# Kernel optimization log

Hardware: AMD Instinct MI355X
Metric: run time of the kernel (lower is better)

## Reference

```python
import jax, jax.numpy as jnp
import numpy as np

N_NODES = 100000

def _graph_conv(x, src, dst, W, b, activation=None):
    # DGL GraphConv with norm='both':
    #   h = D_in^{-1/2} * A^T * (D_out^{-1/2} * x) @ W + b
    n = x.shape[0]
    ones = jnp.ones(src.shape[0], dtype=x.dtype)
    deg_out = jax.ops.segment_sum(ones, src, num_segments=n)
    deg_in = jax.ops.segment_sum(ones, dst, num_segments=n)
    norm_src = jax.lax.rsqrt(jnp.maximum(deg_out, 1.0))  # [N]
    norm_dst = jax.lax.rsqrt(jnp.maximum(deg_in, 1.0))   # [N]
    h = x * norm_src[:, None]
    # DGL applies W before aggregation when out_feats <= in_feats (cheaper messages)
    if W.shape[1] <= W.shape[0]:
        h = h @ W
        agg = jax.ops.segment_sum(h[src], dst, num_segments=n)
    else:
        agg = jax.ops.segment_sum(h[src], dst, num_segments=n)
        agg = agg @ W
    out = agg * norm_dst[:, None] + b
    if activation is not None:
        out = activation(out)
    return out

def setup_inputs() -> dict:
    key = jax.random.key(0)
    k1, k2, k3, k4 = jax.random.split(key, 4)
    in_f, hid_f, out_f = 128, 128, 64
    n_edges = 3200000
    x = jax.random.normal(k1, (N_NODES, in_f), dtype=jnp.float32)
    edge_index = jax.random.randint(k2, (2, n_edges), 0, N_NODES, dtype=jnp.int64)
    W0 = jax.random.normal(k3, (in_f, hid_f), dtype=jnp.float32) / np.sqrt(in_f)
    b0 = jnp.zeros((hid_f,), dtype=jnp.float32)
    W1 = jax.random.normal(k4, (hid_f, out_f), dtype=jnp.float32) / np.sqrt(hid_f)
    b1 = jnp.zeros((out_f,), dtype=jnp.float32)
    return {"x": x, "edge_index": edge_index, "W0": W0, "b0": b0, "W1": W1, "b1": b1}

def reference(x, edge_index, W0, b0, W1, b1):
    src, dst = edge_index[0], edge_index[1]
    h = _graph_conv(x, src, dst, W0, b0, activation=jax.nn.relu)  # gn0: in->hidden, relu
    out = _graph_conv(h, src, dst, W1, b1, activation=None)       # gn1: hidden->out
    return out
```

## Files before the change

kernel.cpp:

```cpp
#include <hip/hip_runtime.h>
#include <hip/hip_bf16.h>


typedef unsigned short u16;
typedef unsigned int   u32;
using bf16x8 = __attribute__((ext_vector_type(8))) short;
using f32x4  = __attribute__((ext_vector_type(4))) float;

__device__ __forceinline__ float bfu2f(u16 u) {
    union { unsigned int i; float f; } c; c.i = ((unsigned int)u) << 16; return c.f;
}
__device__ __forceinline__ u16 f2bfu(float f) {
    union { float fv; unsigned int i; } c; c.fv = f;
    unsigned int x = c.i;
    x += 0x7fffu + ((x >> 16) & 1u);
    return (u16)(x >> 16);
}

constexpr int NCHUNK = 128;

__global__ __launch_bounds__(1024) void hist8_kernel(const int* __restrict__ src,
    const int* __restrict__ dst, int E, int M, u32* __restrict__ pd, u32* __restrict__ ps)
{
    __shared__ u32 h[25088];
    const int W = (M + 3) >> 2;
    const bool isSrc = blockIdx.x >= NCHUNK;
    const int c = isSrc ? (blockIdx.x - NCHUNK) : blockIdx.x;
    const int* vals = isSrc ? src : dst;
    u32* out = (isSrc ? ps : pd) + (size_t)c * W;
    for (int k = threadIdx.x; k < W; k += 1024) h[k] = 0;
    __syncthreads();
    const int ebeg = (int)((long long)c * E / NCHUNK);
    const int eend = (int)((long long)(c + 1) * E / NCHUNK);
    for (int i = ebeg + threadIdx.x; i < eend; i += 1024) {
        int v = vals[i];
        atomicAdd(&h[v >> 2], 1u << ((v & 3) * 8));
    }
    __syncthreads();
    for (int k = threadIdx.x; k < W; k += 1024) out[k] = h[k];
}

__global__ __launch_bounds__(256) void cumreduce_kernel(const u32* __restrict__ pd,
    const u32* __restrict__ ps, u32* __restrict__ cum, int* __restrict__ deg_in,
    float* __restrict__ ns, float* __restrict__ nd, int* __restrict__ bsum, int M)
{
    __shared__ int sh[256];
    const int W = (M + 3) >> 2;
    int w = blockIdx.x * 256 + threadIdx.x;
    u32 run = 0, so = 0;
    if (w < W) {
        for (int c = 0; c < NCHUNK; ++c) {
            cum[(size_t)c * W + w] = run;
            run += pd[(size_t)c * W + w];
        }
        for (int c = 0; c < NCHUNK; ++c) so += ps[(size_t)c * W + w];
        #pragma unroll
        for (int j = 0; j < 4; ++j) {
            int d = w * 4 + j;
            if (d < M) {
                int din  = (run >> (j * 8)) & 255;
                int dout = (so  >> (j * 8)) & 255;
                deg_in[d] = din;
                nd[d] = rsqrtf((float)max(din, 1));
                ns[d] = rsqrtf((float)max(dout, 1));
            }
        }
    }
    sh[threadIdx.x] = (run & 255) + ((run >> 8) & 255) + ((run >> 16) & 255) + (run >> 24);
    __syncthreads();
    for (int off = 128; off > 0; off >>= 1) {
        if (threadIdx.x < off) sh[threadIdx.x] += sh[threadIdx.x + off];
        __syncthreads();
    }
    if (threadIdx.x == 0) bsum[blockIdx.x] = sh[0];
}

__global__ __launch_bounds__(256) void scan2_kernel(const int* __restrict__ bsum,
    int* __restrict__ boff, int NB, int* __restrict__ row_ptr, int M)
{
    __shared__ int sh[256];
    const int t = threadIdx.x;
    sh[t] = (t < NB) ? bsum[t] : 0;
    __syncthreads();
    for (int off = 1; off < 256; off <<= 1) {
        int v = (t >= off) ? sh[t - off] : 0;
        __syncthreads();
        sh[t] += v;
        __syncthreads();
    }
    if (t < NB) boff[t] = (t == 0) ? 0 : sh[t - 1];
    if (t == 0) row_ptr[M] = sh[255];
}

__global__ __launch_bounds__(256) void scan3_kernel(const int* __restrict__ deg,
    const int* __restrict__ boff, int* __restrict__ row_ptr, int M)
{
    __shared__ int sh[256];
    const int base = blockIdx.x * 1024;
    const int idx0 = base + threadIdx.x * 4;
    int v[4]; int s = 0;
    #pragma unroll
    for (int j = 0; j < 4; ++j) {
        int i = idx0 + j;
        v[j] = (i < M) ? deg[i] : 0;
        s += v[j];
    }
    sh[threadIdx.x] = s;
    __syncthreads();
    for (int off = 1; off < 256; off <<= 1) {
        int t = (threadIdx.x >= off) ? sh[threadIdx.x - off] : 0;
        __syncthreads();
        sh[threadIdx.x] += t;
        __syncthreads();
    }
    int run = boff[blockIdx.x] + ((threadIdx.x == 0) ? 0 : sh[threadIdx.x - 1]);
    #pragma unroll
    for (int j = 0; j < 4; ++j) {
        int i = idx0 + j;
        if (i < M) { row_ptr[i] = run; run += v[j]; }
    }
}

constexpr int NS = 8;
__global__ __launch_bounds__(256) void place2_kernel(const int* __restrict__ src,
    const int* __restrict__ dst, int E, int M, const int* __restrict__ row_ptr,
    const u32* __restrict__ cum, int* __restrict__ eidx)
{
    __shared__ u32 rank[3200];
    const int W = (M + 3) >> 2;
    const int r = blockIdx.x >> 7;
    const int c = blockIdx.x & 127;
    const int span = (M + NS - 1) / NS;
    const int lo = r * span;
    const int hi = min(lo + span, M);
    const int wspan = (span + 3) >> 2;
    for (int k = threadIdx.x; k < wspan; k += 256) rank[k] = 0;
    __syncthreads();
    const int ebeg = (int)((long long)c * E / NCHUNK);
    const int eend = (int)((long long)(c + 1) * E / NCHUNK);
    const u32* cumc = cum + (size_t)c * W;
    for (int i = ebeg + threadIdx.x; i < eend; i += 256) {
        int d = dst[i];
        if (d >= lo && d < hi) {
            int dl = d - lo;
            u32 old = atomicAdd(&rank[dl >> 2], 1u << ((dl & 3) * 8));
            int rk   = (old >> ((dl & 3) * 8)) & 255;
            int base = (cumc[d >> 2] >> ((d & 3) * 8)) & 255;
            eidx[row_ptr[d] + base + rk] = src[i];
        }
    }
}

__global__ __launch_bounds__(256) void transpose_kernel(const float* __restrict__ W0,
    const float* __restrict__ W1, u16* __restrict__ Wt0, u16* __restrict__ Wt1)
{
    __shared__ float t[32][33];
    int b = blockIdx.x;
    const float* in; u16* out; int K, N, tk, tn;
    if (b < 16) { in = W0; out = Wt0; K = 128; N = 128; tk = b >> 2; tn = b & 3; }
    else { b -= 16; in = W1; out = Wt1; K = 128; N = 64; tk = b >> 1; tn = b & 1; }
    int tx = threadIdx.x & 31, ty = threadIdx.x >> 5;
    int k0 = tk * 32, n0 = tn * 32;
    #pragma unroll
    for (int i = 0; i < 4; ++i)
        t[ty + 8 * i][tx] = in[(size_t)(k0 + ty + 8 * i) * N + n0 + tx];
    __syncthreads();
    #pragma unroll
    for (int i = 0; i < 4; ++i)
        out[(size_t)(n0 + ty + 8 * i) * K + k0 + tx] = f2bfu(t[tx][ty + 8 * i]);
}

template<int NOUT, bool XF32>
__global__ __launch_bounds__(256) void mfma_gemm_kernel(const void* __restrict__ xin,
    const u16* __restrict__ Wt, const float* __restrict__ rowscale,
    u16* __restrict__ out, int M)
{
    constexpr int CPW = NOUT / 64;
    __shared__ __align__(16) u16 xs[64 * 128];
    __shared__ __align__(16) u16 wl[NOUT * 128];

    const int tid = threadIdx.x;
    const int w = tid >> 6;
    const int l = tid & 63;
    const int ln = l & 15, g = l >> 4;
    const int rbase = blockIdx.x * 64;

    for (int c = tid; c < NOUT * 16; c += 256) {
        int n = c >> 4, s = c & 15;
        uint4 v = *(const uint4*)(Wt + (size_t)n * 128 + s * 8);
        *(uint4*)(&wl[n * 128 + ((s * 8) ^ ((n & 7) << 3))]) = v;
    }
    if (XF32) {
        const float* xf = (const float*)xin;
        for (int c = tid; c < 64 * 16; c += 256) {
            int r = c >> 4, s = c & 15;
            int row = rbase + r;
            uint4 p = make_uint4(0, 0, 0, 0);
            if (row < M) {
                float sc = rowscale[row];
                float4 v0 = *(const float4*)(xf + (size_t)row * 128 + s * 8);
                float4 v1 = *(const float4*)(xf + (size_t)row * 128 + s * 8 + 4);
                p.x = ((u32)f2bfu(v0.y * sc) << 16) | f2bfu(v0.x * sc);
                p.y = ((u32)f2bfu(v0.w * sc) << 16) | f2bfu(v0.z * sc);
                p.z = ((u32)f2bfu(v1.y * sc) << 16) | f2bfu(v1.x * sc);
                p.w = ((u32)f2bfu(v1.w * sc) << 16) | f2bfu(v1.z * sc);
            }
            *(uint4*)(&xs[r * 128 + ((s * 8) ^ ((r & 7) << 3))]) = p;
        }
    } else {
        const u16* xb = (const u16*)xin;
        for (int c = tid; c < 64 * 16; c += 256) {
            int r = c >> 4, s = c & 15;
            int row = rbase + r;
            uint4 v = make_uint4(0, 0, 0, 0);
            if (row < M) v = *(const uint4*)(xb + (size_t)row * 128 + s * 8);
            *(uint4*)(&xs[r * 128 + ((s * 8) ^ ((r & 7) << 3))]) = v;
        }
    }
    __syncthreads();

    bf16x8 bfrag[CPW][4];
    #pragma unroll
    for (int cf = 0; cf < CPW; ++cf) {
        int n = (w * CPW + cf) * 16 + ln;
        #pragma unroll
        for (int ks = 0; ks < 4; ++ks) {
            int koff = ks * 32 + g * 8;
            bfrag[cf][ks] = *(const bf16x8*)(&wl[n * 128 + (koff ^ ((n & 7) << 3))]);
        }
    }

    f32x4 acc[4][CPW];
    #pragma unroll
    for (int m = 0; m < 4; ++m)
        #pragma unroll
        for (int cf = 0; cf < CPW; ++cf)
            acc[m][cf] = (f32x4){0.f, 0.f, 0.f, 0.f};

    #pragma unroll
    for (int m = 0; m < 4; ++m) {
        int r = m * 16 + ln;
        #pragma unroll
        for (int ks = 0; ks < 4; ++ks) {
            int koff = ks * 32 + g * 8;
            bf16x8 a = *(const bf16x8*)(&xs[r * 128 + (koff ^ ((ln & 7) << 3))]);
            #pragma unroll
            for (int cf = 0; cf < CPW; ++cf)
                acc[m][cf] = __builtin_amdgcn_mfma_f32_16x16x32_bf16(
                    a, bfrag[cf][ks], acc[m][cf], 0, 0, 0);
        }
    }

    #pragma unroll
    for (int m = 0; m < 4; ++m) {
        int row = rbase + m * 16 + g * 4;
        #pragma unroll
        for (int j = 0; j < 4; ++j) {
            if (row + j < M) {
                #pragma unroll
                for (int cf = 0; cf < CPW; ++cf) {
                    int col = (w * CPW + cf) * 16 + ln;
                    out[(size_t)(row + j) * NOUT + col] = f2bfu(acc[m][cf][j]);
                }
            }
        }
    }
}

__global__ __launch_bounds__(256) void gather128_kernel(const int* __restrict__ row_ptr,
    const int* __restrict__ eidx, const u16* __restrict__ h,
    const float* __restrict__ nd, const float* __restrict__ nsc,
    const float* __restrict__ b, u16* __restrict__ out, int M)
{
    const int wave = (blockIdx.x * 256 + threadIdx.x) >> 6;
    const int lane = threadIdx.x & 63;
    if (wave >= M) return;
    const int beg = row_ptr[wave];
    const int end = row_ptr[wave + 1];
    const int half = lane >> 5;
    const int l = lane & 31;
    float a0 = 0.f, a1 = 0.f, a2 = 0.f, a3 = 0.f;
    for (int jb = beg; jb < end; jb += 64) {
        const int cnt = min(64, end - jb);
        int myidx = (jb + lane < end) ? eidx[jb + lane] : 0;
        int k = 0;
        for (; k + 8 <= cnt; k += 8) {
            int s0 = __shfl(myidx, k + 0 + half);
            int s1 = __shfl(myidx, k + 2 + half);
            int s2 = __shfl(myidx, k + 4 + half);
            int s3 = __shfl(myidx, k + 6 + half);
            ushort4 u0 = *(const ushort4*)(h + (size_t)s0 * 128 + l * 4);
            ushort4 u1 = *(const ushort4*)(h + (size_t)s1 * 128 + l * 4);
            ushort4 u2 = *(const ushort4*)(h + (size_t)s2 * 128 + l * 4);
            ushort4 u3 = *(const ushort4*)(h + (size_t)s3 * 128 + l * 4);
            a0 += (bfu2f(u0.x) + bfu2f(u1.x)) + (bfu2f(u2.x) + bfu2f(u3.x));
            a1 += (bfu2f(u0.y) + bfu2f(u1.y)) + (bfu2f(u2.y) + bfu2f(u3.y));
            a2 += (bfu2f(u0.z) + bfu2f(u1.z)) + (bfu2f(u2.z) + bfu2f(u3.z));
            a3 += (bfu2f(u0.w) + bfu2f(u1.w)) + (bfu2f(u2.w) + bfu2f(u3.w));
        }
        for (; k < cnt; k += 2) {
            int kk = k + half;
            int s = __shfl(myidx, (kk < cnt) ? kk : 0);
            ushort4 u = *(const ushort4*)(h + (size_t)s * 128 + l * 4);
            if (kk < cnt) {
                a0 += bfu2f(u.x); a1 += bfu2f(u.y);
                a2 += bfu2f(u.z); a3 += bfu2f(u.w);
            }
        }
    }
    a0 += __shfl_xor(a0, 32); a1 += __shfl_xor(a1, 32);
    a2 += __shfl_xor(a2, 32); a3 += __shfl_xor(a3, 32);
    if (half == 0) {
        const float s = nd[wave];
        const float sn = nsc[wave];
        ushort4 o;
        o.x = f2bfu(fmaxf(fmaf(a0, s, b[l * 4 + 0]), 0.f) * sn);
        o.y = f2bfu(fmaxf(fmaf(a1, s, b[l * 4 + 1]), 0.f) * sn);
        o.z = f2bfu(fmaxf(fmaf(a2, s, b[l * 4 + 2]), 0.f) * sn);
        o.w = f2bfu(fmaxf(fmaf(a3, s, b[l * 4 + 3]), 0.f) * sn);
        *(ushort4*)(out + (size_t)wave * 128 + l * 4) = o;
    }
}

__global__ __launch_bounds__(256) void gather64_kernel(const int* __restrict__ row_ptr,
    const int* __restrict__ eidx, const u16* __restrict__ h,
    const float* __restrict__ nd, const float* __restrict__ b,
    float* __restrict__ out, int M)
{
    const int wave = (blockIdx.x * 256 + threadIdx.x) >> 6;
    const int lane = threadIdx.x & 63;
    if (wave >= M) return;
    const int beg = row_ptr[wave];
    const int end = row_ptr[wave + 1];
    const int quad = lane >> 4;
    const int l = lane & 15;
    float a0 = 0.f, a1 = 0.f, a2 = 0.f, a3 = 0.f;
    for (int jb = beg; jb < end; jb += 64) {
        const int cnt = min(64, end - jb);
        int myidx = (jb + lane < end) ? eidx[jb + lane] : 0;
        int k = 0;
        for (; k + 16 <= cnt; k += 16) {
            int s0 = __shfl(myidx, k + 0 + quad);
            int s1 = __shfl(myidx, k + 4 + quad);
            int s2 = __shfl(myidx, k + 8 + quad);
            int s3 = __shfl(myidx, k + 12 + quad);
            ushort4 u0 = *(const ushort4*)(h + (size_t)s0 * 64 + l * 4);
            ushort4 u1 = *(const ushort4*)(h + (size_t)s1 * 64 + l * 4);
            ushort4 u2 = *(const ushort4*)(h + (size_t)s2 * 64 + l * 4);
            ushort4 u3 = *(const ushort4*)(h + (size_t)s3 * 64 + l * 4);
            a0 += (bfu2f(u0.x) + bfu2f(u1.x)) + (bfu2f(u2.x) + bfu2f(u3.x));
            a1 += (bfu2f(u0.y) + bfu2f(u1.y)) + (bfu2f(u2.y) + bfu2f(u3.y));
            a2 += (bfu2f(u0.z) + bfu2f(u1.z)) + (bfu2f(u2.z) + bfu2f(u3.z));
            a3 += (bfu2f(u0.w) + bfu2f(u1.w)) + (bfu2f(u2.w) + bfu2f(u3.w));
        }
        for (; k < cnt; k += 4) {
            int kk = k + quad;
            int s = __shfl(myidx, (kk < cnt) ? kk : 0);
            ushort4 u = *(const ushort4*)(h + (size_t)s * 64 + l * 4);
            if (kk < cnt) {
                a0 += bfu2f(u.x); a1 += bfu2f(u.y);
                a2 += bfu2f(u.z); a3 += bfu2f(u.w);
            }
        }
    }
    a0 += __shfl_xor(a0, 32); a1 += __shfl_xor(a1, 32);
    a2 += __shfl_xor(a2, 32); a3 += __shfl_xor(a3, 32);
    a0 += __shfl_xor(a0, 16); a1 += __shfl_xor(a1, 16);
    a2 += __shfl_xor(a2, 16); a3 += __shfl_xor(a3, 16);
    if (quad == 0) {
        const float s = nd[wave];
        float4 o;
        o.x = fmaf(a0, s, b[l * 4 + 0]);
        o.y = fmaf(a1, s, b[l * 4 + 1]);
        o.z = fmaf(a2, s, b[l * 4 + 2]);
        o.w = fmaf(a3, s, b[l * 4 + 3]);
        *(float4*)(out + (size_t)wave * 64 + l * 4) = o;
    }
}

extern "C" void kernel_launch(void* const* d_in, const int* in_sizes, int n_in,
                              void* d_out, int out_size, void* d_ws, size_t ws_size,
                              hipStream_t stream) {
    const float* x  = (const float*)d_in[0];
    const int*   ei = (const int*)d_in[1];
    const float* W0 = (const float*)d_in[2];
    const float* b0 = (const float*)d_in[3];
    const float* W1 = (const float*)d_in[4];
    const float* b1 = (const float*)d_in[5];

    const int M = in_sizes[0] / 128;
    const int E = in_sizes[1] / 2;
    const int* src = ei;
    const int* dst = ei + E;
    const int W = (M + 3) >> 2;

    char* ws = (char*)d_ws;
    size_t off = 0;
    auto alloc = [&](size_t bytes) {
        void* p = ws + off; off += (bytes + 255) & ~(size_t)255; return p;
    };
    int*   deg_in   = (int*)  alloc((size_t)M * 4);
    float* norm_src = (float*)alloc((size_t)M * 4);
    float* norm_dst = (float*)alloc((size_t)M * 4);
    int*   row_ptr  = (int*)  alloc((size_t)(M + 1) * 4);
    int*   bsum     = (int*)  alloc(256 * 4);
    int*   boff     = (int*)  alloc(256 * 4);
    u16*   Wt0      = (u16*)  alloc(128 * 128 * 2);
    u16*   Wt1      = (u16*)  alloc(64 * 128 * 2);
    int*   eidx     = (int*)  alloc((size_t)E * 4);
    u16*   hbuf     = (u16*)  alloc((size_t)M * 128 * 2);
    u16*   out0b    = (u16*)  alloc((size_t)M * 128 * 2);

    u32* pd  = (u32*)hbuf;
    u32* ps  = pd + (size_t)NCHUNK * W;
    u32* cum = ps + (size_t)NCHUNK * W;

    const int NB = (M + 1023) / 1024;

    hist8_kernel<<<2 * NCHUNK, 1024, 0, stream>>>(src, dst, E, M, pd, ps);
    cumreduce_kernel<<<NB, 256, 0, stream>>>(pd, ps, cum, deg_in,
        norm_src, norm_dst, bsum, M);
    scan2_kernel<<<1, 256, 0, stream>>>(bsum, boff, NB, row_ptr, M);
    scan3_kernel<<<NB, 256, 0, stream>>>(deg_in, boff, row_ptr, M);
    place2_kernel<<<8 * NCHUNK, 256, 0, stream>>>(src, dst, E, M, row_ptr, cum, eidx);
    transpose_kernel<<<24, 256, 0, stream>>>(W0, W1, Wt0, Wt1);

    const int GB = (M + 63) / 64;
    mfma_gemm_kernel<128, true><<<GB, 256, 0, stream>>>(x, Wt0, norm_src, hbuf, M);
    gather128_kernel<<<(M * 64 + 255) / 256, 256, 0, stream>>>(
        row_ptr, eidx, hbuf, norm_dst, norm_src, b0, out0b, M);

    mfma_gemm_kernel<64, false><<<GB, 256, 0, stream>>>(out0b, Wt1, nullptr, hbuf, M);
    gather64_kernel<<<(M * 64 + 255) / 256, 256, 0, stream>>>(
        row_ptr, eidx, hbuf, norm_dst, b1, (float*)d_out, M);
}
```

Before: 309.3 us.

## Widen gather loads to 16-byte bf16x8 and halve place2 destination splits

The two gather kernels now load eight bf16 values per lane as uint4 instead of four as ushort4, so each wave handles twice as many edges per iteration. Each thread keeps eight fp32 accumulators, with an extra shuffle-reduction level at the end. Separately, place2 cuts the destination-range splits from 8 to 4, doubling its LDS rank array, and reorders block-to-chunk mapping so adjacent blocks share edge chunks. The aim is more memory-level parallelism and fewer redundant edge scans, at the cost of more registers and LDS, which may lower occupancy.

```diff
diff --git a/kernel.cpp b/kernel.cpp
--- a/kernel.cpp
+++ b/kernel.cpp
@@ -15,6 +15,17 @@
     unsigned int x = c.i;
     x += 0x7fffu + ((x >> 16) & 1u);
     return (u16)(x >> 16);
+}
+__device__ __forceinline__ void acc8(float* a, uint4 u) {
+    union { u32 i; float f; } c;
+    c.i = u.x << 16;         a[0] += c.f;
+    c.i = u.x & 0xffff0000u; a[1] += c.f;
+    c.i = u.y << 16;         a[2] += c.f;
+    c.i = u.y & 0xffff0000u; a[3] += c.f;
+    c.i = u.z << 16;         a[4] += c.f;
+    c.i = u.z & 0xffff0000u; a[5] += c.f;
+    c.i = u.w << 16;         a[6] += c.f;
+    c.i = u.w & 0xffff0000u; a[7] += c.f;
 }
 
 constexpr int NCHUNK = 128;
@@ -121,15 +132,16 @@
     }
 }
 
-constexpr int NS = 8;
+constexpr int NS = 4;
 __global__ __launch_bounds__(256) void place2_kernel(const int* __restrict__ src,
     const int* __restrict__ dst, int E, int M, const int* __restrict__ row_ptr,
     const u32* __restrict__ cum, int* __restrict__ eidx)
 {
-    __shared__ u32 rank[3200];
+    __shared__ u32 rank[6272];
     const int W = (M + 3) >> 2;
-    const int r = blockIdx.x >> 7;
-    const int c = blockIdx.x & 127;
+    const int bid = blockIdx.x;
+    const int r = (bid & 7) >> 1;
+    const int c = ((bid >> 3) << 1) | (bid & 1);
     const int span = (M + NS - 1) / NS;
     const int lo = r * span;
     const int hi = min(lo + span, M);
@@ -277,48 +289,54 @@
     if (wave >= M) return;
     const int beg = row_ptr[wave];
     const int end = row_ptr[wave + 1];
-    const int half = lane >> 5;
-    const int l = lane & 31;
-    float a0 = 0.f, a1 = 0.f, a2 = 0.f, a3 = 0.f;
+    const int q = lane >> 4;
+    const int l = lane & 15;
+    float a[8] = {};
     for (int jb = beg; jb < end; jb += 64) {
         const int cnt = min(64, end - jb);
         int myidx = (jb + lane < end) ? eidx[jb + lane] : 0;
         int k = 0;
-        for (; k + 8 <= cnt; k += 8) {
-            int s0 = __shfl(myidx, k + 0 + half);
-            int s1 = __shfl(myidx, k + 2 + half);
-            int s2 = __shfl(myidx, k + 4 + half);
-            int s3 = __shfl(myidx, k + 6 + half);
-            ushort4 u0 = *(const ushort4*)(h + (size_t)s0 * 128 + l * 4);
-            ushort4 u1 = *(const ushort4*)(h + (size_t)s1 * 128 + l * 4);
-            ushort4 u2 = *(const ushort4*)(h + (size_t)s2 * 128 + l * 4);
-            ushort4 u3 = *(const ushort4*)(h + (size_t)s3 * 128 + l * 4);
-            a0 += (bfu2f(u0.x) + bfu2f(u1.x)) + (bfu2f(u2.x) + bfu2f(u3.x));
-            a1 += (bfu2f(u0.y) + bfu2f(u1.y)) + (bfu2f(u2.y) + bfu2f(u3.y));
-            a2 += (bfu2f(u0.z) + bfu2f(u1.z)) + (bfu2f(u2.z) + bfu2f(u3.z));
-            a3 += (bfu2f(u0.w) + bfu2f(u1.w)) + (bfu2f(u2.w) + bfu2f(u3.w));
-        }
-        for (; k < cnt; k += 2) {
-            int kk = k + half;
+        for (; k + 16 <= cnt; k += 16) {
+            int s0 = __shfl(myidx, k + 0 + q);
+            int s1 = __shfl(myidx, k + 4 + q);
+            int s2 = __shfl(myidx, k + 8 + q);
+            int s3 = __shfl(myidx, k + 12 + q);
+            uint4 u0 = *(const uint4*)(h + (size_t)s0 * 128 + l * 8);
+            uint4 u1 = *(const uint4*)(h + (size_t)s1 * 128 + l * 8);
+            uint4 u2 = *(const uint4*)(h + (size_t)s2 * 128 + l * 8);
+            uint4 u3 = *(const uint4*)(h + (size_t)s3 * 128 + l * 8);
+            acc8(a, u0); acc8(a, u1); acc8(a, u2); acc8(a, u3);
+        }
+        for (; k < cnt; k += 4) {
+            int kk = k + q;
             int s = __shfl(myidx, (kk < cnt) ? kk : 0);
-            ushort4 u = *(const ushort4*)(h + (size_t)s * 128 + l * 4);
-            if (kk < cnt) {
-                a0 += bfu2f(u.x); a1 += bfu2f(u.y);
-                a2 += bfu2f(u.z); a3 += bfu2f(u.w);
-            }
-        }
-    }
-    a0 += __shfl_xor(a0, 32); a1 += __shfl_xor(a1, 32);
-    a2 += __shfl_xor(a2, 32); a3 += __shfl_xor(a3, 32);
-    if (half == 0) {
+            uint4 u = *(const uint4*)(h + (size_t)s * 128 + l * 8);
+            if (kk < cnt) acc8(a, u);
+        }
+    }
+    #pragma unroll
+    for (int i = 0; i < 8; ++i) {
+        a[i] += __shfl_xor(a[i], 32);
+        a[i] += __shfl_xor(a[i], 16);
+    }
+    if (q == 0) {
         const float s = nd[wave];
         const float sn = nsc[wave];
-        ushort4 o;
-        o.x = f2bfu(fmaxf(fmaf(a0, s, b[l * 4 + 0]), 0.f) * sn);
-        o.y = f2bfu(fmaxf(fmaf(a1, s, b[l * 4 + 1]), 0.f) * sn);
-        o.z = f2bfu(fmaxf(fmaf(a2, s, b[l * 4 + 2]), 0.f) * sn);
-        o.w = f2bfu(fmaxf(fmaf(a3, s, b[l * 4 + 3]), 0.f) * sn);
-        *(ushort4*)(out + (size_t)wave * 128 + l * 4) = o;
+        uint4 o;
+        u32 w0, w1;
+        w0 = f2bfu(fmaxf(fmaf(a[0], s, b[l * 8 + 0]), 0.f) * sn);
+        w1 = f2bfu(fmaxf(fmaf(a[1], s, b[l * 8 + 1]), 0.f) * sn);
+        o.x = (w1 << 16) | w0;
+        w0 = f2bfu(fmaxf(fmaf(a[2], s, b[l * 8 + 2]), 0.f) * sn);
+        w1 = f2bfu(fmaxf(fmaf(a[3], s, b[l * 8 + 3]), 0.f) * sn);
+        o.y = (w1 << 16) | w0;
+        w0 = f2bfu(fmaxf(fmaf(a[4], s, b[l * 8 + 4]), 0.f) * sn);
+        w1 = f2bfu(fmaxf(fmaf(a[5], s, b[l * 8 + 5]), 0.f) * sn);
+        o.z = (w1 << 16) | w0;
+        w0 = f2bfu(fmaxf(fmaf(a[6], s, b[l * 8 + 6]), 0.f) * sn);
+        w1 = f2bfu(fmaxf(fmaf(a[7], s, b[l * 8 + 7]), 0.f) * sn);
+        o.w = (w1 << 16) | w0;
+        *(uint4*)(out + (size_t)wave * 128 + l * 8) = o;
     }
 }
 
@@ -332,49 +350,50 @@
     if (wave >= M) return;
     const int beg = row_ptr[wave];
     const int end = row_ptr[wave + 1];
-    const int quad = lane >> 4;
-    const int l = lane & 15;
-    float a0 = 0.f, a1 = 0.f, a2 = 0.f, a3 = 0.f;
+    const int o = lane >> 3;
+    const int l = lane & 7;
+    float a[8] = {};
     for (int jb = beg; jb < end; jb += 64) {
         const int cnt = min(64, end - jb);
         int myidx = (jb + lane < end) ? eidx[jb + lane] : 0;
         int k = 0;
-        for (; k + 16 <= cnt; k += 16) {
-            int s0 = __shfl(myidx, k + 0 + quad);
-            int s1 = __shfl(myidx, k + 4 + quad);
-            int s2 = __shfl(myidx, k + 8 + quad);
-            int s3 = __shfl(myidx, k + 12 + quad);
-            ushort4 u0 = *(const ushort4*)(h + (size_t)s0 * 64 + l * 4);
-            ushort4 u1 = *(const ushort4*)(h + (size_t)s1 * 64 + l * 4);
-            ushort4 u2 = *(const ushort4*)(h + (size_t)s2 * 64 + l * 4);
-            ushort4 u3 = *(const ushort4*)(h + (size_t)s3 * 64 + l * 4);
-            a0 += (bfu2f(u0.x) + bfu2f(u1.x)) + (bfu2f(u2.x) + bfu2f(u3.x));
-            a1 += (bfu2f(u0.y) + bfu2f(u1.y)) + (bfu2f(u2.y) + bfu2f(u3.y));
-            a2 += (bfu2f(u0.z) + bfu2f(u1.z)) + (bfu2f(u2.z) + bfu2f(u3.z));
-            a3 += (bfu2f(u0.w) + bfu2f(u1.w)) + (bfu2f(u2.w) + bfu2f(u3.w));
-        }
-        for (; k < cnt; k += 4) {
-            int kk = k + quad;
+        for (; k + 32 <= cnt; k += 32) {
+            int s0 = __shfl(myidx, k + 0 + o);
+            int s1 = __shfl(myidx, k + 8 + o);
+            int s2 = __shfl(myidx, k + 16 + o);
+            int s3 = __shfl(myidx, k + 24 + o);
+            uint4 u0 = *(const uint4*)(h + (size_t)s0 * 64 + l * 8);
+            uint4 u1 = *(const uint4*)(h + (size_t)s1 * 64 + l * 8);
+            uint4 u2 = *(const uint4*)(h + (size_t)s2 * 64 + l * 8);
+            uint4 u3 = *(const uint4*)(h + (size_t)s3 * 64 + l * 8);
+            acc8(a, u0); acc8(a, u1); acc8(a, u2); acc8(a, u3);
+        }
+        for (; k < cnt; k += 8) {
+            int kk = k + o;
             int s = __shfl(myidx, (kk < cnt) ? kk : 0);
-            ushort4 u = *(const ushort4*)(h + (size_t)s * 64 + l * 4);
-            if (kk < cnt) {
-                a0 += bfu2f(u.x); a1 += bfu2f(u.y);
-                a2 += bfu2f(u.z); a3 += bfu2f(u.w);
-            }
-        }
-    }
-    a0 += __shfl_xor(a0, 32); a1 += __shfl_xor(a1, 32);
-    a2 += __shfl_xor(a2, 32); a3 += __shfl_xor(a3, 32);
-    a0 += __shfl_xor(a0, 16); a1 += __shfl_xor(a1, 16);
-    a2 += __shfl_xor(a2, 16); a3 += __shfl_xor(a3, 16);
-    if (quad == 0) {
+            uint4 u = *(const uint4*)(h + (size_t)s * 64 + l * 8);
+            if (kk < cnt) acc8(a, u);
+        }
+    }
+    #pragma unroll
+    for (int i = 0; i < 8; ++i) {
+        a[i] += __shfl_xor(a[i], 32);
+        a[i] += __shfl_xor(a[i], 16);
+        a[i] += __shfl_xor(a[i], 8);
+    }
+    if (o == 0) {
         const float s = nd[wave];
-        float4 o;
-        o.x = fmaf(a0, s, b[l * 4 + 0]);
-        o.y = fmaf(a1, s, b[l * 4 + 1]);
-        o.z = fmaf(a2, s, b[l * 4 + 2]);
-        o.w = fmaf(a3, s, b[l * 4 + 3]);
-        *(float4*)(out + (size_t)wave * 64 + l * 4) = o;
+        float4 o0, o1;
+        o0.x = fmaf(a[0], s, b[l * 8 + 0]);
+        o0.y = fmaf(a[1], s, b[l * 8 + 1]);
+        o0.z = fmaf(a[2], s, b[l * 8 + 2]);
+        o0.w = fmaf(a[3], s, b[l * 8 + 3]);
+        o1.x = fmaf(a[4], s, b[l * 8 + 4]);
+        o1.y = fmaf(a[5], s, b[l * 8 + 5]);
+        o1.z = fmaf(a[6], s, b[l * 8 + 6]);
+        o1.w = fmaf(a[7], s, b[l * 8 + 7]);
+        *(float4*)(out + (size_t)wave * 64 + l * 8) = o0;
+        *(float4*)(out + (size_t)wave * 64 + l * 8 + 4) = o1;
     }
 }
 
@@ -422,7 +441,7 @@
         norm_src, norm_dst, bsum, M);
     scan2_kernel<<<1, 256, 0, stream>>>(bsum, boff, NB, row_ptr, M);
     scan3_kernel<<<NB, 256, 0, stream>>>(deg_in, boff, row_ptr, M);
-    place2_kernel<<<8 * NCHUNK, 256, 0, stream>>>(src, dst, E, M, row_ptr, cum, eidx);
+    place2_kernel<<<NS * NCHUNK, 256, 0, stream>>>(src, dst, E, M, row_ptr, cum, eidx);
     transpose_kernel<<<24, 256, 0, stream>>>(W0, W1, Wt0, Wt1);
 
     const int GB = (M + 63) / 64;
```

New measurement: 307.5 us. Within noise of the previous version (-0.6%).
